# Kernel optimization log

Hardware: AMD Instinct MI355X
Metric: run time of the kernel (lower is better)

## Reference

```python
import jax, jax.numpy as jnp
import numpy as np

H = 1024
VOCAB = 32000


def setup_inputs() -> dict:
    key = jax.random.key(0)
    ks = jax.random.split(key, 16)
    N, B, T = 32, 64, 400
    s = 1.0 / np.sqrt(H)
    inp = {
        "input_seq": jax.random.randint(ks[0], (N, B), 0, VOCAB),
        "last_hidden": jax.random.normal(ks[1], (1, B, H), jnp.float32),
        "encoder_outputs": jax.random.normal(ks[2], (T, B, H), jnp.float32),
        "encoderB_outputs": jax.random.normal(ks[3], (T, B, H), jnp.float32),
        # parameters
        "emb": jax.random.normal(ks[4], (VOCAB, H), jnp.float32),
        "W_ih": jax.random.uniform(ks[5], (3 * H, H), jnp.float32, -s, s),
        "W_hh": jax.random.uniform(ks[6], (3 * H, H), jnp.float32, -s, s),
        "b_ih": jax.random.uniform(ks[7], (3 * H,), jnp.float32, -s, s),
        "b_hh": jax.random.uniform(ks[8], (3 * H,), jnp.float32, -s, s),
        "attn_W": jax.random.uniform(ks[9], (H, 2 * H), jnp.float32, -s, s),
        "attn_b": jax.random.uniform(ks[10], (H,), jnp.float32, -s, s),
        "attn_v": jax.random.uniform(ks[11], (H,), jnp.float32, -s, s),
        "concat_W": jax.random.uniform(ks[12], (H, 3 * H), jnp.float32, -s, s),
        "concat_b": jax.random.uniform(ks[13], (H,), jnp.float32, -s, s),
        "out_W": jax.random.uniform(ks[14], (VOCAB, H), jnp.float32, -s, s),
        "out_b": jax.random.uniform(ks[15], (VOCAB,), jnp.float32, -s, s),
    }
    return inp


def _gru(x, h0, W_ih, W_hh, b_ih, b_hh):
    # x: (N,B,H), h0: (B,H). PyTorch GRU cell equations.
    def step(h, x_t):
        gi = x_t @ W_ih.T + b_ih          # (B,3H)
        gh = h @ W_hh.T + b_hh
        i_r, i_z, i_n = jnp.split(gi, 3, axis=-1)
        h_r, h_z, h_n = jnp.split(gh, 3, axis=-1)
        r = jax.nn.sigmoid(i_r + h_r)
        z = jax.nn.sigmoid(i_z + h_z)
        n = jnp.tanh(i_n + r * h_n)
        h_new = (1.0 - z) * n + z * h
        return h_new, h_new
    hN, outs = jax.lax.scan(step, h0, x)
    return outs, hN


def _attention(rnn_out, enc, attn_W, attn_b, v):
    # score(h, e) = (Linear([h; e]) ) . v  -- linear in both, so separable.
    W1, W2 = attn_W[:, :H], attn_W[:, H:]
    u1 = W1.T @ v                         # (H,)
    u2 = W2.T @ v
    bias = attn_b @ v                     # scalar
    a = rnn_out @ u1                      # (N,B)
    c = enc @ u2 + bias                   # (T,B)
    # energies (B,N,T), softmax over T (matches F.softmax on (-1, max_len))
    e = a.T[:, :, None] + c.T[:, None, :]
    w = jax.nn.softmax(e, axis=-1)        # (B,N,T)
    ctx = jnp.einsum('bnt,tbh->nbh', w, enc)  # bmm then transpose(0,1)
    return w, ctx


def reference(input_seq, last_hidden, encoder_outputs, encoderB_outputs,
              emb, W_ih, W_hh, b_ih, b_hh, attn_W, attn_b, attn_v,
              concat_W, concat_b, out_W, out_b):
    x = emb[input_seq]                                   # (N,B,H)
    rnn_out, hN = _gru(x, last_hidden[0], W_ih, W_hh, b_ih, b_hh)
    hidden = hN[None]                                    # (1,B,H)
    uw, u_ctx = _attention(rnn_out, encoder_outputs, attn_W, attn_b, attn_v)
    bw, b_ctx = _attention(rnn_out, encoderB_outputs, attn_W, attn_b, attn_v)
    cat = jnp.concatenate([rnn_out, u_ctx, b_ctx], axis=2)   # (N,B,3H)
    h = jnp.tanh(cat @ concat_W.T + concat_b)
    output = h @ out_W.T + out_b                          # (N,B,VOCAB)
    return output, hidden, uw, bw
```

## Files before the change

### kernel.cpp

```cpp
#include <hip/hip_runtime.h>
#include <cstdint>
#include <cstddef>

namespace {

constexpr int kH  = 1024;
constexpr int kB  = 64;
constexpr int kN  = 32;
constexpr int kT  = 400;
constexpr int kV  = 32000;
constexpr int kM  = kN * kB;
constexpr int k3H = 3 * kH;

typedef _Float16 f16;
typedef _Float16 f16x4 __attribute__((ext_vector_type(4)));
typedef _Float16 f16x8 __attribute__((ext_vector_type(8)));
typedef float    f32x4v __attribute__((ext_vector_type(4)));

__device__ __forceinline__ void gload_lds16(const void* g, void* l) {
  __builtin_amdgcn_global_load_lds((__attribute__((address_space(1))) void*)g,
                                   (__attribute__((address_space(3))) void*)l,
                                   16, 0, 0);
}

__device__ __forceinline__ uint32_t pack_f16x2(f16 lo, f16 hi) {
  union { f16 h[2]; uint32_t u; } c;
  c.h[0] = lo; c.h[1] = hi;
  return c.u;
}


__global__ void cvt_f16_kernel(const float* __restrict__ src, f16* __restrict__ dst, int n4) {
  int i = blockIdx.x * blockDim.x + threadIdx.x;
  const int stride = gridDim.x * blockDim.x;
  for (; i < n4; i += stride) {
    float4 v = reinterpret_cast<const float4*>(src)[i];
    f16x4 o = { (f16)v.x, (f16)v.y, (f16)v.z, (f16)v.w };
    reinterpret_cast<f16x4*>(dst)[i] = o;
  }
}

__global__ void gather_x_kernel(const int* __restrict__ seq, const float* __restrict__ emb,
                                f16* __restrict__ xh) {
  const int m = blockIdx.x;
  const int tok = seq[m];
  float4 v = reinterpret_cast<const float4*>(emb + (size_t)tok * kH)[threadIdx.x];
  f16x4 o = { (f16)v.x, (f16)v.y, (f16)v.z, (f16)v.w };
  reinterpret_cast<f16x4*>(xh + (size_t)m * kH)[threadIdx.x] = o;
}

__global__ void init_h_kernel(const float* __restrict__ lh, f16* __restrict__ hh0) {
  const int i = blockIdx.x * blockDim.x + threadIdx.x;
  float4 v = reinterpret_cast<const float4*>(lh)[i];
  f16x4 o = { (f16)v.x, (f16)v.y, (f16)v.z, (f16)v.w };
  reinterpret_cast<f16x4*>(hh0)[i] = o;
}

__global__ void attn_prep_kernel(const float* __restrict__ attn_W, const float* __restrict__ attn_b,
                                 const float* __restrict__ v, float* __restrict__ u2,
                                 float* __restrict__ biasS) {
  const int h = blockIdx.x;
  const int lane = threadIdx.x;
  float sum = 0.0f;
  if (h < kH) {
    for (int k = lane; k < kH; k += 64)
      sum += attn_W[(size_t)k * (2 * kH) + kH + h] * v[k];
  } else {
    for (int k = lane; k < kH; k += 64)
      sum += attn_b[k] * v[k];
  }
  #pragma unroll
  for (int o = 32; o > 0; o >>= 1) sum += __shfl_xor(sum, o);
  if (lane == 0) {
    if (h < kH) u2[h] = sum; else biasS[0] = sum;
  }
}


template <bool TANH, bool NT, typename OUT_T>
__global__ __launch_bounds__(256)
void gemm_bt_kernel(const f16* __restrict__ A, const f16* __restrict__ Bt,
                    const float* __restrict__ bias, OUT_T* __restrict__ C,
                    int M, int N, int K) {
  __shared__ __align__(16) f16 As[128 * 64];
  __shared__ __align__(16) f16 Bs[128 * 64];
  const int tid  = threadIdx.x;
  const int wave = tid >> 6;
  const int lane = tid & 63;
  const int m0 = blockIdx.x * 128;
  const int n0 = blockIdx.y * 128;
  const int wm = (wave >> 1) * 64;
  const int wn = (wave & 1) * 64;
  const int rsub = lane >> 3;
  const int coff = (lane & 7) * 8;
  f32x4v acc[4][4] = {};
  const int nk = K >> 6;
  for (int kc = 0; kc < nk; ++kc) {
    const f16* Ag = A + (size_t)m0 * K + kc * 64;
    const f16* Bg = Bt + (size_t)n0 * K + kc * 64;
    for (int c = wave; c < 16; c += 4) {
      const int row = c * 8 + rsub;
      gload_lds16(Ag + (size_t)row * K + coff, &As[c * 512]);
      gload_lds16(Bg + (size_t)row * K + coff, &Bs[c * 512]);
    }
    __syncthreads();
    #pragma unroll
    for (int kk = 0; kk < 2; ++kk) {
      const int ko = kk * 32 + (lane >> 4) * 8;
      f16x8 af[4], bfr[4];
      #pragma unroll
      for (int i = 0; i < 4; ++i) {
        af[i]  = *reinterpret_cast<const f16x8*>(&As[(wm + i * 16 + (lane & 15)) * 64 + ko]);
        bfr[i] = *reinterpret_cast<const f16x8*>(&Bs[(wn + i * 16 + (lane & 15)) * 64 + ko]);
      }
      #pragma unroll
      for (int mi = 0; mi < 4; ++mi)
        #pragma unroll
        for (int ni = 0; ni < 4; ++ni)
          acc[mi][ni] = __builtin_amdgcn_mfma_f32_16x16x32_f16(af[mi], bfr[ni], acc[mi][ni], 0, 0, 0);
    }
    __syncthreads();
  }
  const int rb = (lane >> 4) * 4;
  const int cb = lane & 15;
  #pragma unroll
  for (int mi = 0; mi < 4; ++mi) {
    #pragma unroll
    for (int ni = 0; ni < 4; ++ni) {
      const int col = n0 + wn + ni * 16 + cb;
      const float bv = bias[col];
      #pragma unroll
      for (int r = 0; r < 4; ++r) {
        const int row = m0 + wm + mi * 16 + rb + r;
        float v = acc[mi][ni][r] + bv;
        if (TANH) v = tanhf(v);
        if (NT) __builtin_nontemporal_store((OUT_T)v, &C[(size_t)row * N + col]);
        else C[(size_t)row * N + col] = (OUT_T)v;
      }
    }
  }
}


constexpr int kGruBlks = 64;
constexpr int kAttnBlks = 128;
constexpr int kCvtBlks = 320;
constexpr int kMegaBlks = kGruBlks + kAttnBlks + kCvtBlks;

__global__ __launch_bounds__(256, 1)
void mega_kernel(const f16* __restrict__ Whh, const float* __restrict__ bhh,
                 const float* __restrict__ gi, const float* __restrict__ lh,
                 f16* __restrict__ HHa, f16* __restrict__ HHb,
                 f16* __restrict__ cath, float* __restrict__ hiddenOut,
                 unsigned int* __restrict__ flags,
                 const float* __restrict__ enc0, const float* __restrict__ enc1,
                 const float* __restrict__ u2, const float* __restrict__ biasS,
                 float* __restrict__ uw, float* __restrict__ bw,
                 const float* __restrict__ oW, f16* __restrict__ oWh,
                 const float* __restrict__ cW, f16* __restrict__ cWh) {
  __shared__ union SM {
    float ghp[4][64][52];
    struct { float4 u2s[256]; float srow[kT]; float red[8]; } at;
  } sm;
  const int bid = blockIdx.x;
  const int tid = threadIdx.x;

  if (bid < kGruBlks) {
    const int wave = tid >> 6;
    const int lane = tid & 63;
    const int ln   = lane & 15;
    const int khi  = lane >> 4;
    const int j0   = bid * 16;
    const int kw   = wave * 256;
    const int fm   = tid >> 2;
    const int fc   = (tid & 3) * 4;
    const int myprod = wave * 16 + ln;

    f16x8 bfr[3][8];
    #pragma unroll
    for (int s = 0; s < 3; ++s)
      #pragma unroll
      for (int ks = 0; ks < 8; ++ks)
        bfr[s][ks] = *reinterpret_cast<const f16x8*>(
            &Whh[(size_t)(s * kH + j0 + ln) * kH + kw + ks * 32 + khi * 8]);

    float hreg[4], bR[4], bZ[4], bN[4];
    #pragma unroll
    for (int e = 0; e < 4; ++e) {
      const int j = j0 + fc + e;
      hreg[e] = lh[(size_t)fm * kH + j];
      bR[e] = bhh[j]; bZ[e] = bhh[kH + j]; bN[e] = bhh[2 * kH + j];
    }

    for (int step = 0; step < kN; ++step) {
      const f16* hh  = (step & 1) ? HHb : HHa;
      f16*       hho = (step & 1) ? HHa : HHb;

      float4 giL[3];
      {
        const size_t mm = (size_t)step * kB + fm;
        #pragma unroll
        for (int s = 0; s < 3; ++s)
          giL[s] = *reinterpret_cast<const float4*>(&gi[mm * k3H + s * kH + j0 + fc]);
      }

      if (step > 0) {
        while (true) {
          unsigned int f = __hip_atomic_load(&flags[myprod], __ATOMIC_RELAXED,
                                             __HIP_MEMORY_SCOPE_SYSTEM);
          if (__all(f >= (unsigned int)step)) break;
          __builtin_amdgcn_s_sleep(1);
        }
        __builtin_amdgcn_fence(__ATOMIC_ACQUIRE, "agent");
      }

      f16x8 af[8][4];
      #pragma unroll
      for (int ks = 0; ks < 8; ++ks)
        #pragma unroll
        for (int mi = 0; mi < 4; ++mi)
          af[ks][mi] = *reinterpret_cast<const f16x8*>(
              &hh[(size_t)(mi * 16 + ln) * kH + kw + ks * 32 + khi * 8]);

      f32x4v acc[4][3] = {};
      #pragma unroll
      for (int ks = 0; ks < 8; ++ks)
        #pragma unroll
        for (int mi = 0; mi < 4; ++mi)
          #pragma unroll
          for (int s = 0; s < 3; ++s)
            acc[mi][s] = __builtin_amdgcn_mfma_f32_16x16x32_f16(af[ks][mi], bfr[s][ks], acc[mi][s], 0, 0, 0);

      #pragma unroll
      for (int mi = 0; mi < 4; ++mi)
        #pragma unroll
        for (int s = 0; s < 3; ++s)
          #pragma unroll
          for (int r = 0; r < 4; ++r)
            sm.ghp[wave][mi * 16 + khi * 4 + r][s * 16 + ln] = acc[mi][s][r];
      __syncthreads();

      float4 gr4 = {0,0,0,0}, gz4 = {0,0,0,0}, gn4 = {0,0,0,0};
      #pragma unroll
      for (int w = 0; w < 4; ++w) {
        float4 a = *reinterpret_cast<const float4*>(&sm.ghp[w][fm][fc]);
        float4 b = *reinterpret_cast<const float4*>(&sm.ghp[w][fm][16 + fc]);
        float4 c = *reinterpret_cast<const float4*>(&sm.ghp[w][fm][32 + fc]);
        gr4.x += a.x; gr4.y += a.y; gr4.z += a.z; gr4.w += a.w;
        gz4.x += b.x; gz4.y += b.y; gz4.z += b.z; gz4.w += b.w;
        gn4.x += c.x; gn4.y += c.y; gn4.z += c.z; gn4.w += c.w;
      }
      float hv[4];
      const float* grp = &gr4.x; const float* gzp = &gz4.x; const float* gnp = &gn4.x;
      const float* gil0 = &giL[0].x; const float* gil1 = &giL[1].x; const float* gil2 = &giL[2].x;
      #pragma unroll
      for (int e = 0; e < 4; ++e) {
        const float r  = 1.0f / (1.0f + expf(-(gil0[e] + grp[e] + bR[e])));
        const float z  = 1.0f / (1.0f + expf(-(gil1[e] + gzp[e] + bZ[e])));
        const float nn = tanhf(gil2[e] + r * (gnp[e] + bN[e]));
        hv[e] = (1.0f - z) * nn + z * hreg[e];
        hreg[e] = hv[e];
      }
      const uint32_t p01 = pack_f16x2((f16)hv[0], (f16)hv[1]);
      const uint32_t p23 = pack_f16x2((f16)hv[2], (f16)hv[3]);
      const unsigned long long pk64 = (unsigned long long)p01 | ((unsigned long long)p23 << 32);
      __hip_atomic_store(reinterpret_cast<unsigned long long*>(&hho[(size_t)fm * kH + j0 + fc]),
                         pk64, __ATOMIC_RELAXED, __HIP_MEMORY_SCOPE_AGENT);
      __syncthreads();
      if (step < kN - 1 && tid == 0)
        __hip_atomic_store(&flags[bid], (unsigned int)(step + 1),
                           __ATOMIC_RELAXED, __HIP_MEMORY_SCOPE_SYSTEM);
      uint2 pku; pku.x = p01; pku.y = p23;
      *reinterpret_cast<uint2*>(&cath[((size_t)step * kB + fm) * k3H + j0 + fc]) = pku;
      if (step == kN - 1) {
        float4 hv4 = { hv[0], hv[1], hv[2], hv[3] };
        *reinterpret_cast<float4*>(&hiddenOut[(size_t)fm * kH + j0 + fc]) = hv4;
      }
    }
  } else if (bid < kGruBlks + kAttnBlks) {
    const int idx = bid - kGruBlks;
    const int e = idx >> 6, b = idx & 63;
    const float* enc = e ? enc1 : enc0;
    const int wave = tid >> 6, lane = tid & 63;

    sm.at.u2s[tid] = *reinterpret_cast<const float4*>(&u2[tid * 4]);
    __syncthreads();
    const float bias = biasS[0];

    for (int t = wave; t < kT; t += 4) {
      const float* row = enc + ((size_t)t * kB + b) * kH + lane * 16;
      float s = 0.0f;
      #pragma unroll
      for (int i = 0; i < 4; ++i) {
        float4 ev = reinterpret_cast<const float4*>(row)[i];
        float4 uv = sm.at.u2s[lane * 4 + i];
        s += ev.x * uv.x + ev.y * uv.y + ev.z * uv.z + ev.w * uv.w;
      }
      #pragma unroll
      for (int o = 32; o > 0; o >>= 1) s += __shfl_xor(s, o);
      if (lane == 0) sm.at.srow[t] = s + bias;
    }
    __syncthreads();

    float lmax = -1e30f;
    for (int t = tid; t < kT; t += 256) lmax = fmaxf(lmax, sm.at.srow[t]);
    #pragma unroll
    for (int o = 32; o > 0; o >>= 1) lmax = fmaxf(lmax, __shfl_xor(lmax, o));
    if (lane == 0) sm.at.red[wave] = lmax;
    __syncthreads();
    const float m = fmaxf(fmaxf(sm.at.red[0], sm.at.red[1]), fmaxf(sm.at.red[2], sm.at.red[3]));
    float lsum = 0.0f;
    for (int t = tid; t < kT; t += 256) {
      float ev = expf(sm.at.srow[t] - m);
      sm.at.srow[t] = ev;
      lsum += ev;
    }
    #pragma unroll
    for (int o = 32; o > 0; o >>= 1) lsum += __shfl_xor(lsum, o);
    if (lane == 0) sm.at.red[4 + wave] = lsum;
    __syncthreads();
    const float inv = 1.0f / (sm.at.red[4] + sm.at.red[5] + sm.at.red[6] + sm.at.red[7]);
    for (int t = tid; t < kT; t += 256) sm.at.srow[t] *= inv;
    __syncthreads();

    float* outp = (e ? bw : uw) + (size_t)b * kN * kT;
    for (int n = 0; n < kN; ++n)
      for (int t = tid; t < kT; t += 256)
        __builtin_nontemporal_store(sm.at.srow[t], &outp[n * kT + t]);

    const int j = tid * 4;
    float4 acc = {0,0,0,0};
    for (int t = 0; t < kT; ++t) {
      const float wt = sm.at.srow[t];
      const float4 ev = *reinterpret_cast<const float4*>(&enc[((size_t)t * kB + b) * kH + j]);
      acc.x += wt * ev.x; acc.y += wt * ev.y; acc.z += wt * ev.z; acc.w += wt * ev.w;
    }
    f16x4 cv = { (f16)acc.x, (f16)acc.y, (f16)acc.z, (f16)acc.w };
    #pragma unroll
    for (int n = 0; n < kN; ++n)
      *reinterpret_cast<f16x4*>(&cath[((size_t)(n * kB + b)) * k3H + kH + e * kH + j]) = cv;
  } else {
    constexpr int nOW = kV * kH / 4;
    constexpr int nCW = kH * k3H / 4;
    const int stride = kCvtBlks * 256;
    for (int i = (bid - kGruBlks - kAttnBlks) * 256 + tid; i < nOW + nCW; i += stride) {
      if (i < nOW) {
        float4 v = reinterpret_cast<const float4*>(oW)[i];
        f16x4 o = { (f16)v.x, (f16)v.y, (f16)v.z, (f16)v.w };
        reinterpret_cast<f16x4*>(oWh)[i] = o;
      } else {
        const int k = i - nOW;
        float4 v = reinterpret_cast<const float4*>(cW)[k];
        f16x4 o = { (f16)v.x, (f16)v.y, (f16)v.z, (f16)v.w };
        reinterpret_cast<f16x4*>(cWh)[k] = o;
      }
    }
  }
}

}


extern "C" void kernel_launch(void* const* d_in, const int* in_sizes, int n_in,
                              void* d_out, int out_size, void* d_ws, size_t ws_size,
                              hipStream_t stream) {
  (void)in_sizes; (void)n_in; (void)out_size; (void)ws_size;
  const int*   seq    = (const int*)d_in[0];
  const float* lh     = (const float*)d_in[1];
  const float* enc0   = (const float*)d_in[2];
  const float* enc1   = (const float*)d_in[3];
  const float* emb    = (const float*)d_in[4];
  const float* W_ih   = (const float*)d_in[5];
  const float* W_hh   = (const float*)d_in[6];
  const float* b_ih   = (const float*)d_in[7];
  const float* b_hh   = (const float*)d_in[8];
  const float* attn_W = (const float*)d_in[9];
  const float* attn_b = (const float*)d_in[10];
  const float* attn_v = (const float*)d_in[11];
  const float* cW     = (const float*)d_in[12];
  const float* cb     = (const float*)d_in[13];
  const float* oW     = (const float*)d_in[14];
  const float* ob     = (const float*)d_in[15];
  float* out = (float*)d_out;

  char* ws = (char*)d_ws;
  constexpr size_t oWih = 0;
  constexpr size_t oWhh = oWih + 6291456;
  constexpr size_t oCW  = oWhh + 6291456;
  constexpr size_t oOW  = oCW + 6291456;
  constexpr size_t oX   = oOW + 65536000;
  constexpr size_t oGI  = oX + 4194304;
  constexpr size_t oH0  = oGI + 25165824;
  constexpr size_t oH1  = oH0 + 262144;
  constexpr size_t oHH0 = oH1 + 262144;
  constexpr size_t oHH1 = oHH0 + 131072;
  constexpr size_t oCAT = oHH1 + 131072;
  constexpr size_t oH2  = oCAT + 12582912;
  constexpr size_t oU2  = oH2 + 4194304;
  constexpr size_t oBS  = oU2 + 4096;
  constexpr size_t oC   = oBS + 256;
  constexpr size_t oWSM = oC + 204800;
  constexpr size_t oCTR = oWSM + 204800;

  f16*   Wih_h = (f16*)(ws + oWih);
  f16*   Whh_h = (f16*)(ws + oWhh);
  f16*   cW_h  = (f16*)(ws + oCW);
  f16*   oW_h  = (f16*)(ws + oOW);
  f16*   X_h   = (f16*)(ws + oX);
  float* GI    = (float*)(ws + oGI);
  f16*   HH0   = (f16*)(ws + oHH0);
  f16*   HH1   = (f16*)(ws + oHH1);
  f16*   CAT   = (f16*)(ws + oCAT);
  f16*   H2    = (f16*)(ws + oH2);
  float* U2    = (float*)(ws + oU2);
  float* BS    = (float*)(ws + oBS);
  unsigned int* FLAGS = (unsigned int*)(ws + oCTR);

  constexpr size_t oHidden = (size_t)kM * kV;
  constexpr size_t oUW = oHidden + (size_t)kB * kH;
  constexpr size_t oBW = oUW + (size_t)kB * kN * kT;

  cvt_f16_kernel<<<1024, 256, 0, stream>>>(W_ih, Wih_h, k3H * kH / 4);
  cvt_f16_kernel<<<1024, 256, 0, stream>>>(W_hh, Whh_h, k3H * kH / 4);
  gather_x_kernel<<<kM, 256, 0, stream>>>(seq, emb, X_h);
  init_h_kernel<<<64, 256, 0, stream>>>(lh, HH0);
  attn_prep_kernel<<<1025, 64, 0, stream>>>(attn_W, attn_b, attn_v, U2, BS);
  hipMemsetAsync(FLAGS, 0, 64 * sizeof(unsigned int), stream);

  gemm_bt_kernel<false, false, float><<<dim3(16, 24), 256, 0, stream>>>(X_h, Wih_h, b_ih, GI, kM, k3H, kH);

  mega_kernel<<<kMegaBlks, 256, 0, stream>>>(Whh_h, b_hh, GI, lh, HH0, HH1, CAT,
                                             out + oHidden, FLAGS,
                                             enc0, enc1, U2, BS,
                                             out + oUW, out + oBW,
                                             oW, oW_h, cW, cW_h);

  gemm_bt_kernel<true, false, f16><<<dim3(16, 8), 256, 0, stream>>>(CAT, cW_h, cb, H2, kM, kH, k3H);
  gemm_bt_kernel<false, true, float><<<dim3(16, 250), 256, 0, stream>>>(H2, oW_h, ob, out, kM, kV, kH);
}
```

Before: 691.4 us.

## Fuse concat and output GEMMs into persistent mega kernel with flag-driven pipelining

Merges the small prep kernels into one pre_kernel and moves the concat (tanh) GEMM and the vocab output GEMM into the persistent mega_kernel. Non-GRU blocks convert weights, compute attention, then run concat row tiles as soon as enough GRU steps are done, followed by output tiles gated on per-row counters. The goal is to overlap the serial GRU recurrence with the large GEMMs and to remove launch gaps. In exchange it adds spin-waits and atomic stores, and with 256 worker blocks versus the full-grid GEMM there is risk of lower throughput or deadlock if blocks are not all co-resident.

```diff
diff --git a/kernel.cpp b/kernel.cpp
--- a/kernel.cpp
+++ b/kernel.cpp
@@ -29,58 +29,70 @@
   return c.u;
 }
 
-
-__global__ void cvt_f16_kernel(const float* __restrict__ src, f16* __restrict__ dst, int n4) {
-  int i = blockIdx.x * blockDim.x + threadIdx.x;
-  const int stride = gridDim.x * blockDim.x;
-  for (; i < n4; i += stride) {
-    float4 v = reinterpret_cast<const float4*>(src)[i];
-    f16x4 o = { (f16)v.x, (f16)v.y, (f16)v.z, (f16)v.w };
-    reinterpret_cast<f16x4*>(dst)[i] = o;
-  }
-}
-
-__global__ void gather_x_kernel(const int* __restrict__ seq, const float* __restrict__ emb,
-                                f16* __restrict__ xh) {
-  const int m = blockIdx.x;
-  const int tok = seq[m];
-  float4 v = reinterpret_cast<const float4*>(emb + (size_t)tok * kH)[threadIdx.x];
-  f16x4 o = { (f16)v.x, (f16)v.y, (f16)v.z, (f16)v.w };
-  reinterpret_cast<f16x4*>(xh + (size_t)m * kH)[threadIdx.x] = o;
-}
-
-__global__ void init_h_kernel(const float* __restrict__ lh, f16* __restrict__ hh0) {
-  const int i = blockIdx.x * blockDim.x + threadIdx.x;
-  float4 v = reinterpret_cast<const float4*>(lh)[i];
-  f16x4 o = { (f16)v.x, (f16)v.y, (f16)v.z, (f16)v.w };
-  reinterpret_cast<f16x4*>(hh0)[i] = o;
-}
-
-__global__ void attn_prep_kernel(const float* __restrict__ attn_W, const float* __restrict__ attn_b,
-                                 const float* __restrict__ v, float* __restrict__ u2,
-                                 float* __restrict__ biasS) {
-  const int h = blockIdx.x;
-  const int lane = threadIdx.x;
-  float sum = 0.0f;
-  if (h < kH) {
-    for (int k = lane; k < kH; k += 64)
-      sum += attn_W[(size_t)k * (2 * kH) + kH + h] * v[k];
+constexpr int C_FLAGS = 0;
+constexpr int C_CVT   = 64;
+constexpr int C_ATTN  = 80;
+constexpr int C_CONC  = 96;
+
+constexpr int NOUT = 16 * 250;
+
+
+__global__ __launch_bounds__(256)
+void pre_kernel(const float* __restrict__ Wih, f16* __restrict__ WihH,
+                const float* __restrict__ Whh, f16* __restrict__ WhhH,
+                const int* __restrict__ seq, const float* __restrict__ emb,
+                f16* __restrict__ Xh, const float* __restrict__ lh,
+                f16* __restrict__ HH0,
+                const float* __restrict__ attnW, const float* __restrict__ attnB,
+                const float* __restrict__ attnV,
+                float* __restrict__ u2, float* __restrict__ biasS) {
+  const int bid = blockIdx.x, tid = threadIdx.x;
+  if (bid < 512) {
+    const float* src = (bid < 256) ? Wih : Whh;
+    f16* dst = (bid < 256) ? WihH : WhhH;
+    constexpr int n4 = k3H * kH / 4;
+    for (int i = (bid & 255) * 256 + tid; i < n4; i += 256 * 256) {
+      float4 v = reinterpret_cast<const float4*>(src)[i];
+      f16x4 o = { (f16)v.x, (f16)v.y, (f16)v.z, (f16)v.w };
+      reinterpret_cast<f16x4*>(dst)[i] = o;
+    }
+  } else if (bid < 640) {
+    const int m0 = (bid - 512) * 16;
+    for (int k = 0; k < 16; ++k) {
+      const int m = m0 + k;
+      const int tok = seq[m];
+      float4 v = reinterpret_cast<const float4*>(emb + (size_t)tok * kH)[tid];
+      f16x4 o = { (f16)v.x, (f16)v.y, (f16)v.z, (f16)v.w };
+      reinterpret_cast<f16x4*>(Xh + (size_t)m * kH)[tid] = o;
+    }
+  } else if (bid < 644) {
+    for (int i = (bid - 640) * 256 + tid; i < 16384; i += 1024) {
+      float4 v = reinterpret_cast<const float4*>(lh)[i];
+      f16x4 o = { (f16)v.x, (f16)v.y, (f16)v.z, (f16)v.w };
+      reinterpret_cast<f16x4*>(HH0)[i] = o;
+    }
   } else {
-    for (int k = lane; k < kH; k += 64)
-      sum += attn_b[k] * v[k];
-  }
-  #pragma unroll
-  for (int o = 32; o > 0; o >>= 1) sum += __shfl_xor(sum, o);
-  if (lane == 0) {
-    if (h < kH) u2[h] = sum; else biasS[0] = sum;
-  }
-}
-
-
-template <bool TANH, bool NT, typename OUT_T>
+    const int item = (bid - 644) * 4 + (tid >> 6);
+    const int lane = tid & 63;
+    if (item > kH) return;
+    float sum = 0.0f;
+    if (item < kH) {
+      for (int k = lane; k < kH; k += 64)
+        sum += attnW[(size_t)k * (2 * kH) + kH + item] * attnV[k];
+    } else {
+      for (int k = lane; k < kH; k += 64)
+        sum += attnB[k] * attnV[k];
+    }
+    #pragma unroll
+    for (int o = 32; o > 0; o >>= 1) sum += __shfl_xor(sum, o);
+    if (lane == 0) { if (item < kH) u2[item] = sum; else biasS[0] = sum; }
+  }
+}
+
+
 __global__ __launch_bounds__(256)
 void gemm_bt_kernel(const f16* __restrict__ A, const f16* __restrict__ Bt,
-                    const float* __restrict__ bias, OUT_T* __restrict__ C,
+                    const float* __restrict__ bias, float* __restrict__ C,
                     int M, int N, int K) {
   __shared__ __align__(16) f16 As[128 * 64];
   __shared__ __align__(16) f16 Bs[128 * 64];
@@ -124,50 +136,126 @@
   const int rb = (lane >> 4) * 4;
   const int cb = lane & 15;
   #pragma unroll
-  for (int mi = 0; mi < 4; ++mi) {
+  for (int mi = 0; mi < 4; ++mi)
     #pragma unroll
     for (int ni = 0; ni < 4; ++ni) {
       const int col = n0 + wn + ni * 16 + cb;
       const float bv = bias[col];
       #pragma unroll
-      for (int r = 0; r < 4; ++r) {
-        const int row = m0 + wm + mi * 16 + rb + r;
-        float v = acc[mi][ni][r] + bv;
-        if (TANH) v = tanhf(v);
-        if (NT) __builtin_nontemporal_store((OUT_T)v, &C[(size_t)row * N + col]);
-        else C[(size_t)row * N + col] = (OUT_T)v;
-      }
-    }
-  }
-}
-
-
-constexpr int kGruBlks = 64;
-constexpr int kAttnBlks = 128;
-constexpr int kCvtBlks = 320;
-constexpr int kMegaBlks = kGruBlks + kAttnBlks + kCvtBlks;
+      for (int r = 0; r < 4; ++r)
+        C[(size_t)(m0 + wm + mi * 16 + rb + r) * N + col] = acc[mi][ni][r] + bv;
+    }
+}
+
+
+union SMem {
+  float ghp[4][64][52];
+  struct { float4 u2s[256]; float srow[kT]; float red[8]; } at;
+  struct { __align__(16) f16 As[128 * 64]; __align__(16) f16 Bs[128 * 64]; } st;
+};
+
+template <int MODE>
+__device__ void work_tile(SMem& sm, const f16* __restrict__ Ag0, const f16* __restrict__ Bg0,
+                          const float* __restrict__ bias, void* __restrict__ Cout,
+                          int K, int m0, int n0) {
+  const int tid  = threadIdx.x;
+  const int wave = tid >> 6;
+  const int lane = tid & 63;
+  const int wm = (wave >> 1) * 64;
+  const int wn = (wave & 1) * 64;
+  const int rsub = lane >> 3;
+  const int coff = (lane & 7) * 8;
+  f32x4v acc[4][4] = {};
+  const int nk = K >> 6;
+  for (int kc = 0; kc < nk; ++kc) {
+    const f16* Ag = Ag0 + kc * 64;
+    const f16* Bg = Bg0 + kc * 64;
+    for (int c = wave; c < 16; c += 4) {
+      const int row = c * 8 + rsub;
+      gload_lds16(Ag + (size_t)row * K + coff, &sm.st.As[c * 512]);
+      gload_lds16(Bg + (size_t)row * K + coff, &sm.st.Bs[c * 512]);
+    }
+    __syncthreads();
+    #pragma unroll
+    for (int kk = 0; kk < 2; ++kk) {
+      const int ko = kk * 32 + (lane >> 4) * 8;
+      f16x8 af[4], bfr[4];
+      #pragma unroll
+      for (int i = 0; i < 4; ++i) {
+        af[i]  = *reinterpret_cast<const f16x8*>(&sm.st.As[(wm + i * 16 + (lane & 15)) * 64 + ko]);
+        bfr[i] = *reinterpret_cast<const f16x8*>(&sm.st.Bs[(wn + i * 16 + (lane & 15)) * 64 + ko]);
+      }
+      #pragma unroll
+      for (int mi = 0; mi < 4; ++mi)
+        #pragma unroll
+        for (int ni = 0; ni < 4; ++ni)
+          acc[mi][ni] = __builtin_amdgcn_mfma_f32_16x16x32_f16(af[mi], bfr[ni], acc[mi][ni], 0, 0, 0);
+    }
+    __syncthreads();
+  }
+  const int rb = (lane >> 4) * 4;
+  const int cb = lane & 15;
+  if (MODE == 0) {
+    f16* tile = sm.st.As;
+    #pragma unroll
+    for (int mi = 0; mi < 4; ++mi)
+      #pragma unroll
+      for (int ni = 0; ni < 4; ++ni) {
+        const int col = wn + ni * 16 + cb;
+        const float bv = bias[n0 + col];
+        #pragma unroll
+        for (int r = 0; r < 4; ++r)
+          tile[(wm + mi * 16 + rb + r) * 128 + col] = (f16)tanhf(acc[mi][ni][r] + bv);
+      }
+    __syncthreads();
+    f16* H2 = (f16*)Cout;
+    const int row = tid >> 1;
+    const int c0  = (tid & 1) * 64;
+    #pragma unroll
+    for (int i = 0; i < 16; ++i) {
+      union { f16x4 v; unsigned long long u; } cv;
+      cv.v = *reinterpret_cast<const f16x4*>(&tile[row * 128 + c0 + i * 4]);
+      __hip_atomic_store(reinterpret_cast<unsigned long long*>(
+          &H2[(size_t)(m0 + row) * kH + n0 + c0 + i * 4]),
+          cv.u, __ATOMIC_RELAXED, __HIP_MEMORY_SCOPE_AGENT);
+    }
+  } else {
+    float* C = (float*)Cout;
+    #pragma unroll
+    for (int mi = 0; mi < 4; ++mi)
+      #pragma unroll
+      for (int ni = 0; ni < 4; ++ni) {
+        const int col = n0 + wn + ni * 16 + cb;
+        const float bv = bias[col];
+        #pragma unroll
+        for (int r = 0; r < 4; ++r)
+          __builtin_nontemporal_store(acc[mi][ni][r] + bv,
+              &C[(size_t)(m0 + wm + mi * 16 + rb + r) * kV + col]);
+      }
+  }
+}
 
 __global__ __launch_bounds__(256, 1)
 void mega_kernel(const f16* __restrict__ Whh, const float* __restrict__ bhh,
                  const float* __restrict__ gi, const float* __restrict__ lh,
                  f16* __restrict__ HHa, f16* __restrict__ HHb,
                  f16* __restrict__ cath, float* __restrict__ hiddenOut,
-                 unsigned int* __restrict__ flags,
+                 unsigned int* __restrict__ ctr,
                  const float* __restrict__ enc0, const float* __restrict__ enc1,
                  const float* __restrict__ u2, const float* __restrict__ biasS,
                  float* __restrict__ uw, float* __restrict__ bw,
                  const float* __restrict__ oW, f16* __restrict__ oWh,
-                 const float* __restrict__ cW, f16* __restrict__ cWh) {
-  __shared__ union SM {
-    float ghp[4][64][52];
-    struct { float4 u2s[256]; float srow[kT]; float red[8]; } at;
-  } sm;
+                 const float* __restrict__ cW, f16* __restrict__ cWh,
+                 const float* __restrict__ cb, const float* __restrict__ ob,
+                 f16* __restrict__ H2, float* __restrict__ outC) {
+  __shared__ SMem sm;
   const int bid = blockIdx.x;
   const int tid = threadIdx.x;
-
-  if (bid < kGruBlks) {
-    const int wave = tid >> 6;
-    const int lane = tid & 63;
+  const int wave = tid >> 6;
+  const int lane = tid & 63;
+  unsigned int* flags = ctr + C_FLAGS;
+
+  if (bid < 64) {
     const int ln   = lane & 15;
     const int khi  = lane >> 4;
     const int j0   = bid * 16;
@@ -252,12 +340,12 @@
       }
       float hv[4];
       const float* grp = &gr4.x; const float* gzp = &gz4.x; const float* gnp = &gn4.x;
-      const float* gil0 = &giL[0].x; const float* gil1 = &giL[1].x; const float* gil2 = &giL[2].x;
+      const float* g0 = &giL[0].x; const float* g1 = &giL[1].x; const float* g2 = &giL[2].x;
       #pragma unroll
       for (int e = 0; e < 4; ++e) {
-        const float r  = 1.0f / (1.0f + expf(-(gil0[e] + grp[e] + bR[e])));
-        const float z  = 1.0f / (1.0f + expf(-(gil1[e] + gzp[e] + bZ[e])));
-        const float nn = tanhf(gil2[e] + r * (gnp[e] + bN[e]));
+        const float r  = 1.0f / (1.0f + expf(-(g0[e] + grp[e] + bR[e])));
+        const float z  = 1.0f / (1.0f + expf(-(g1[e] + gzp[e] + bZ[e])));
+        const float nn = tanhf(g2[e] + r * (gnp[e] + bN[e]));
         hv[e] = (1.0f - z) * nn + z * hreg[e];
         hreg[e] = hv[e];
       }
@@ -266,22 +354,46 @@
       const unsigned long long pk64 = (unsigned long long)p01 | ((unsigned long long)p23 << 32);
       __hip_atomic_store(reinterpret_cast<unsigned long long*>(&hho[(size_t)fm * kH + j0 + fc]),
                          pk64, __ATOMIC_RELAXED, __HIP_MEMORY_SCOPE_AGENT);
+      __hip_atomic_store(reinterpret_cast<unsigned long long*>(
+                         &cath[((size_t)step * kB + fm) * k3H + j0 + fc]),
+                         pk64, __ATOMIC_RELAXED, __HIP_MEMORY_SCOPE_AGENT);
       __syncthreads();
-      if (step < kN - 1 && tid == 0)
+      if (tid == 0)
         __hip_atomic_store(&flags[bid], (unsigned int)(step + 1),
                            __ATOMIC_RELAXED, __HIP_MEMORY_SCOPE_SYSTEM);
-      uint2 pku; pku.x = p01; pku.y = p23;
-      *reinterpret_cast<uint2*>(&cath[((size_t)step * kB + fm) * k3H + j0 + fc]) = pku;
       if (step == kN - 1) {
         float4 hv4 = { hv[0], hv[1], hv[2], hv[3] };
         *reinterpret_cast<float4*>(&hiddenOut[(size_t)fm * kH + j0 + fc]) = hv4;
       }
     }
-  } else if (bid < kGruBlks + kAttnBlks) {
-    const int idx = bid - kGruBlks;
-    const int e = idx >> 6, b = idx & 63;
+    return;
+  }
+
+  {
+    constexpr int nOW = kV * kH / 4;
+    constexpr int nCW = kH * k3H / 4;
+    const int wb = bid - 64;
+    for (int i = wb * 256 + tid; i < nOW + nCW; i += 256 * 256) {
+      const float4 v = (i < nOW) ? reinterpret_cast<const float4*>(oW)[i]
+                                 : reinterpret_cast<const float4*>(cW)[i - nOW];
+      union { f16x4 h; unsigned long long u; } cv;
+      cv.h = (f16x4){ (f16)v.x, (f16)v.y, (f16)v.z, (f16)v.w };
+      unsigned long long* dst = (i < nOW)
+          ? reinterpret_cast<unsigned long long*>(oWh) + i
+          : reinterpret_cast<unsigned long long*>(cWh) + (i - nOW);
+      __hip_atomic_store(dst, cv.u, __ATOMIC_RELAXED, __HIP_MEMORY_SCOPE_AGENT);
+    }
+    __syncthreads();
+    if (tid == 0)
+      __hip_atomic_fetch_add(&ctr[C_CVT], 1u, __ATOMIC_RELAXED, __HIP_MEMORY_SCOPE_SYSTEM);
+  }
+
+  const int w = bid - 64;
+  const bool isAttn = (w < 128);
+
+  if (isAttn) {
+    const int e = w >> 6, b = w & 63;
     const float* enc = e ? enc1 : enc0;
-    const int wave = tid >> 6, lane = tid & 63;
 
     sm.at.u2s[tid] = *reinterpret_cast<const float4*>(&u2[tid * 4]);
     __syncthreads();
@@ -335,26 +447,81 @@
       const float4 ev = *reinterpret_cast<const float4*>(&enc[((size_t)t * kB + b) * kH + j]);
       acc.x += wt * ev.x; acc.y += wt * ev.y; acc.z += wt * ev.z; acc.w += wt * ev.w;
     }
-    f16x4 cv = { (f16)acc.x, (f16)acc.y, (f16)acc.z, (f16)acc.w };
+    union { f16x4 h; unsigned long long u; } cv;
+    cv.h = (f16x4){ (f16)acc.x, (f16)acc.y, (f16)acc.z, (f16)acc.w };
     #pragma unroll
     for (int n = 0; n < kN; ++n)
-      *reinterpret_cast<f16x4*>(&cath[((size_t)(n * kB + b)) * k3H + kH + e * kH + j]) = cv;
-  } else {
-    constexpr int nOW = kV * kH / 4;
-    constexpr int nCW = kH * k3H / 4;
-    const int stride = kCvtBlks * 256;
-    for (int i = (bid - kGruBlks - kAttnBlks) * 256 + tid; i < nOW + nCW; i += stride) {
-      if (i < nOW) {
-        float4 v = reinterpret_cast<const float4*>(oW)[i];
-        f16x4 o = { (f16)v.x, (f16)v.y, (f16)v.z, (f16)v.w };
-        reinterpret_cast<f16x4*>(oWh)[i] = o;
-      } else {
-        const int k = i - nOW;
-        float4 v = reinterpret_cast<const float4*>(cW)[k];
-        f16x4 o = { (f16)v.x, (f16)v.y, (f16)v.z, (f16)v.w };
-        reinterpret_cast<f16x4*>(cWh)[k] = o;
-      }
-    }
+      __hip_atomic_store(reinterpret_cast<unsigned long long*>(
+          &cath[((size_t)(n * kB + b)) * k3H + kH + e * kH + j]),
+          cv.u, __ATOMIC_RELAXED, __HIP_MEMORY_SCOPE_AGENT);
+    __syncthreads();
+    if (tid == 0)
+      __hip_atomic_fetch_add(&ctr[C_ATTN], 1u, __ATOMIC_RELAXED, __HIP_MEMORY_SCOPE_SYSTEM);
+    __syncthreads();
+  }
+
+  const int rci    = isAttn ? (w >> 3) : 0;
+  const int climit = isAttn ? rci * 250 : 0;
+  int lastReady = -1;
+  int o = w;
+
+  for (; o < climit; o += 256) {
+    const int r = o / 250, ct = o % 250;
+    if (r > lastReady) {
+      if (tid == 0)
+        while (__hip_atomic_load(&ctr[C_CONC + 16 * r], __ATOMIC_RELAXED,
+                                 __HIP_MEMORY_SCOPE_SYSTEM) < 8u)
+          __builtin_amdgcn_s_sleep(16);
+      __syncthreads();
+      __builtin_amdgcn_fence(__ATOMIC_ACQUIRE, "agent");
+      lastReady = r;
+    }
+    work_tile<1>(sm, H2 + (size_t)(128 * r) * kH, oWh + (size_t)(128 * ct) * kH,
+                 ob, outC, kH, 128 * r, 128 * ct);
+    __syncthreads();
+  }
+
+  if (isAttn) {
+    const int cct = w & 7;
+    if (wave == 0) {
+      const unsigned int tgt = 2 * rci + 2;
+      while (true) {
+        unsigned int f = __hip_atomic_load(&flags[lane], __ATOMIC_RELAXED,
+                                           __HIP_MEMORY_SCOPE_SYSTEM);
+        if (__all(f >= tgt)) break;
+        __builtin_amdgcn_s_sleep(16);
+      }
+    }
+    if (tid == 0) {
+      while (__hip_atomic_load(&ctr[C_ATTN], __ATOMIC_RELAXED, __HIP_MEMORY_SCOPE_SYSTEM) < 128u)
+        __builtin_amdgcn_s_sleep(16);
+      while (__hip_atomic_load(&ctr[C_CVT], __ATOMIC_RELAXED, __HIP_MEMORY_SCOPE_SYSTEM) < 256u)
+        __builtin_amdgcn_s_sleep(16);
+    }
+    __syncthreads();
+    __builtin_amdgcn_fence(__ATOMIC_ACQUIRE, "agent");
+    work_tile<0>(sm, cath + (size_t)(128 * rci) * k3H, cWh + (size_t)(128 * cct) * k3H,
+                 cb, H2, k3H, 128 * rci, 128 * cct);
+    __syncthreads();
+    if (tid == 0)
+      __hip_atomic_fetch_add(&ctr[C_CONC + 16 * rci], 1u,
+                             __ATOMIC_RELAXED, __HIP_MEMORY_SCOPE_SYSTEM);
+  }
+
+  for (; o < NOUT; o += 256) {
+    const int r = o / 250, ct = o % 250;
+    if (r > lastReady) {
+      if (tid == 0)
+        while (__hip_atomic_load(&ctr[C_CONC + 16 * r], __ATOMIC_RELAXED,
+                                 __HIP_MEMORY_SCOPE_SYSTEM) < 8u)
+          __builtin_amdgcn_s_sleep(16);
+      __syncthreads();
+      __builtin_amdgcn_fence(__ATOMIC_ACQUIRE, "agent");
+      lastReady = r;
+    }
+    work_tile<1>(sm, H2 + (size_t)(128 * r) * kH, oWh + (size_t)(128 * ct) * kH,
+                 ob, outC, kH, 128 * r, 128 * ct);
+    __syncthreads();
   }
 }
 
@@ -390,17 +557,13 @@
   constexpr size_t oOW  = oCW + 6291456;
   constexpr size_t oX   = oOW + 65536000;
   constexpr size_t oGI  = oX + 4194304;
-  constexpr size_t oH0  = oGI + 25165824;
-  constexpr size_t oH1  = oH0 + 262144;
-  constexpr size_t oHH0 = oH1 + 262144;
+  constexpr size_t oHH0 = oGI + 25165824;
   constexpr size_t oHH1 = oHH0 + 131072;
   constexpr size_t oCAT = oHH1 + 131072;
   constexpr size_t oH2  = oCAT + 12582912;
   constexpr size_t oU2  = oH2 + 4194304;
   constexpr size_t oBS  = oU2 + 4096;
-  constexpr size_t oC   = oBS + 256;
-  constexpr size_t oWSM = oC + 204800;
-  constexpr size_t oCTR = oWSM + 204800;
+  constexpr size_t oCTR = oBS + 256;
 
   f16*   Wih_h = (f16*)(ws + oWih);
   f16*   Whh_h = (f16*)(ws + oWhh);
@@ -414,27 +577,22 @@
   f16*   H2    = (f16*)(ws + oH2);
   float* U2    = (float*)(ws + oU2);
   float* BS    = (float*)(ws + oBS);
-  unsigned int* FLAGS = (unsigned int*)(ws + oCTR);
+  unsigned int* CTR = (unsigned int*)(ws + oCTR);
 
   constexpr size_t oHidden = (size_t)kM * kV;
   constexpr size_t oUW = oHidden + (size_t)kB * kH;
   constexpr size_t oBW = oUW + (size_t)kB * kN * kT;
 
-  cvt_f16_kernel<<<1024, 256, 0, stream>>>(W_ih, Wih_h, k3H * kH / 4);
-  cvt_f16_kernel<<<1024, 256, 0, stream>>>(W_hh, Whh_h, k3H * kH / 4);
-  gather_x_kernel<<<kM, 256, 0, stream>>>(seq, emb, X_h);
-  init_h_kernel<<<64, 256, 0, stream>>>(lh, HH0);
-  attn_prep_kernel<<<1025, 64, 0, stream>>>(attn_W, attn_b, attn_v, U2, BS);
-  hipMemsetAsync(FLAGS, 0, 64 * sizeof(unsigned int), stream);
-
-  gemm_bt_kernel<false, false, float><<<dim3(16, 24), 256, 0, stream>>>(X_h, Wih_h, b_ih, GI, kM, k3H, kH);
-
-  mega_kernel<<<kMegaBlks, 256, 0, stream>>>(Whh_h, b_hh, GI, lh, HH0, HH1, CAT,
-                                             out + oHidden, FLAGS,
-                                             enc0, enc1, U2, BS,
-                                             out + oUW, out + oBW,
-                                             oW, oW_h, cW, cW_h);
-
-  gemm_bt_kernel<true, false, f16><<<dim3(16, 8), 256, 0, stream>>>(CAT, cW_h, cb, H2, kM, kH, k3H);
-  gemm_bt_kernel<false, true, float><<<dim3(16, 250), 256, 0, stream>>>(H2, oW_h, ob, out, kM, kV, kH);
-}
+  pre_kernel<<<901, 256, 0, stream>>>(W_ih, Wih_h, W_hh, Whh_h, seq, emb, X_h,
+                                      lh, HH0, attn_W, attn_b, attn_v, U2, BS);
+  hipMemsetAsync(CTR, 0, 4096, stream);
+
+  gemm_bt_kernel<<<dim3(16, 24), 256, 0, stream>>>(X_h, Wih_h, b_ih, GI, kM, k3H, kH);
+
+  mega_kernel<<<320, 256, 0, stream>>>(Whh_h, b_hh, GI, lh, HH0, HH1, CAT,
+                                       out + oHidden, CTR,
+                                       enc0, enc1, U2, BS,
+                                       out + oUW, out + oBW,
+                                       oW, oW_h, cW, cW_h,
+                                       cb, ob, H2, out);
+}
```

Result: slower. 2.270 ms (+228.3%).
